# Kernel tuning notes

Measured on AMD Instinct MI355X. Metric: run time of the kernel, lower is better.

## Reference

```python
import jax, jax.numpy as jnp
import numpy as np


def _grid_sample_3d(vol, pts):
    """Trilinear grid_sample, align_corners=True, padding_mode='border'.
    vol: [C, D, H, W]; pts: [N, 3] with (x, y, z) in normalized [-1, 1] coords
    (x indexes W, y indexes H, z indexes D, matching torch.grid_sample).
    Returns [N, C]."""
    C, D, H, W = vol.shape
    def to_idx(c, size):
        c = (c + 1.0) * 0.5 * (size - 1)
        return jnp.clip(c, 0.0, size - 1.0)  # border padding
    ix = to_idx(pts[:, 0], W)
    iy = to_idx(pts[:, 1], H)
    iz = to_idx(pts[:, 2], D)
    x0 = jnp.floor(ix); y0 = jnp.floor(iy); z0 = jnp.floor(iz)
    wx = ix - x0;       wy = iy - y0;       wz = iz - z0
    x0i = x0.astype(jnp.int32); x1i = jnp.minimum(x0i + 1, W - 1)
    y0i = y0.astype(jnp.int32); y1i = jnp.minimum(y0i + 1, H - 1)
    z0i = z0.astype(jnp.int32); z1i = jnp.minimum(z0i + 1, D - 1)
    g = lambda zi, yi, xi: vol[:, zi, yi, xi]  # [C, N]
    out = (g(z0i, y0i, x0i) * (1 - wz) * (1 - wy) * (1 - wx)
         + g(z0i, y0i, x1i) * (1 - wz) * (1 - wy) * wx
         + g(z0i, y1i, x0i) * (1 - wz) * wy * (1 - wx)
         + g(z0i, y1i, x1i) * (1 - wz) * wy * wx
         + g(z1i, y0i, x0i) * wz * (1 - wy) * (1 - wx)
         + g(z1i, y0i, x1i) * wz * (1 - wy) * wx
         + g(z1i, y1i, x0i) * wz * wy * (1 - wx)
         + g(z1i, y1i, x1i) * wz * wy * wx)
    return out.T  # [N, C]


def _skinning(x, w, tfs):
    """x: [B,N,3], w: [B,N,J], tfs: [B,J,4,4] -> (xd [B,N,3], w_tf [B,N,4,4])."""
    x_h = jnp.concatenate([x, jnp.ones_like(x[..., :1])], axis=-1)  # [B,N,4]
    w_tf = jnp.einsum('bpn,bnij->bpij', w, tfs)                      # [B,N,4,4]
    xh = jnp.einsum('bpij,bpj->bpi', w_tf, x_h)                      # [B,N,4]
    return xh[..., :3], w_tf


def setup_inputs() -> dict:
    key = jax.random.key(0)
    ks = jax.random.split(key, 12)
    B, N, J = 4, 250000, 55
    return {
        'xc': jax.random.normal(ks[0], (B, N, 3), jnp.float32),
        'shape_offset': jax.random.normal(ks[1], (B, N, 3), jnp.float32),
        'pose_offset': jax.random.normal(ks[2], (B, N, 3), jnp.float32),
        'tfs': jax.random.normal(ks[3], (B, J, 4, 4), jnp.float32),
        'tfs_inv': jax.random.normal(ks[4], (1, J, 4, 4), jnp.float32),
        'poseoff_ori': jax.random.normal(ks[5], (1, N, 3), jnp.float32),
        'lbsw': jax.random.uniform(ks[6], (1, N, J), jnp.float32),
        'mask': jax.random.randint(ks[7], (1, N), 0, 2).astype(bool),
        'lbs_voxel': jax.random.uniform(ks[8], (1, J, 16, 64, 64), jnp.float32),
        'offset_kernel': jnp.zeros((1, 1, 3), jnp.float32),
        'scale_kernel': jax.random.uniform(ks[9], (1, 1, 3), jnp.float32),
    }


def reference(xc, shape_offset, pose_offset, tfs, tfs_inv, poseoff_ori,
              lbsw, mask, lbs_voxel, offset_kernel, scale_kernel):
    B = xc.shape[0]
    # query_weights: normalize then trilinear grid sample of shared voxel
    xn = (xc + offset_kernel) * scale_kernel  # [B,N,3]
    vol = lbs_voxel[0]                        # [J,16,64,64], shared across batch
    w = jax.vmap(lambda p: _grid_sample_3d(vol, p))(xn)  # [B,N,J]
    # w[:, mask[0]] = lbsw[mask]
    w = jnp.where(mask[0][None, :, None], lbsw, w)
    # first blend: canonical with tfs_inv (inverse=False path)
    xc_cano, w_tf_inv = _skinning(xc, w, jnp.broadcast_to(tfs_inv, (B,) + tfs_inv.shape[1:]))
    xc_cano_ori = xc_cano - poseoff_ori
    xc_shape = xc_cano_ori + shape_offset + pose_offset
    # second blend: posed with tfs
    xd, w_tf = _skinning(xc_shape, w, tfs)
    w_tf_all = w_tf @ w_tf_inv  # [B,N,4,4] batched 4x4 matmul
    return xd, w_tf_all
```

## Files before the change

kernel.cpp:

```cpp
#include <hip/hip_runtime.h>
#include <hip/hip_fp16.h>


#define JNT 55
#define VD  16
#define VH  64
#define VW  64
#define NVOX (VD * VH * VW)

typedef float f4u __attribute__((ext_vector_type(4), aligned(4)));

__global__ __launch_bounds__(256) void build_tab_k(
    const float* __restrict__ vol, const float* __restrict__ tfs,
    const float* __restrict__ tfs_inv, __half* __restrict__ tab)
{
    int v = blockIdx.x * 256 + threadIdx.x;
    int b = blockIdx.y;
    if (v >= NVOX) return;

    float Mi[16], Mv[16];
#pragma unroll
    for (int i = 0; i < 16; ++i) { Mi[i] = 0.f; Mv[i] = 0.f; }
    const float* tb = tfs + (size_t)b * JNT * 16;
#pragma unroll 1
    for (int j = 0; j < JNT; ++j) {
        float wj = vol[j * NVOX + v];
#pragma unroll
        for (int i = 0; i < 16; ++i) Mi[i] = fmaf(wj, tfs_inv[j * 16 + i], Mi[i]);
#pragma unroll
        for (int i = 0; i < 16; ++i) Mv[i] = fmaf(wj, tb[j * 16 + i], Mv[i]);
    }
    float h[16];
#pragma unroll
    for (int i = 0; i < 8; ++i)
        h[i] = __builtin_bit_cast(float, __floats2half2_rn(Mi[2*i], Mi[2*i+1]));
#pragma unroll
    for (int i = 0; i < 8; ++i)
        h[8+i] = __builtin_bit_cast(float, __floats2half2_rn(Mv[2*i], Mv[2*i+1]));

    float4* d4 = (float4*)(tab + ((size_t)b * NVOX + v) * 32);
    d4[0] = make_float4(h[0],  h[1],  h[2],  h[3]);
    d4[1] = make_float4(h[4],  h[5],  h[6],  h[7]);
    d4[2] = make_float4(h[8],  h[9],  h[10], h[11]);
    d4[3] = make_float4(h[12], h[13], h[14], h[15]);
}

__device__ __forceinline__ void acc8(float cw, float4 r, float* a)
{
    float rr[4] = {r.x, r.y, r.z, r.w};
#pragma unroll
    for (int kk = 0; kk < 4; ++kk) {
        __half2 h = __builtin_bit_cast(__half2, rr[kk]);
        float2 f = __half22float2(h);
        a[2*kk]     = fmaf(cw, f.x, a[2*kk]);
        a[2*kk + 1] = fmaf(cw, f.y, a[2*kk + 1]);
    }
}

__device__ __forceinline__ void epilogue(
    int b, int n, int N, float x, float y, float z,
    const float* A, const float* Ai,
    const float* __restrict__ shoff, const float* __restrict__ pooff,
    const float* __restrict__ poori,
    float* __restrict__ out_xd, float* __restrict__ out_w)
{
    size_t pid = (size_t)b * N + n;
    size_t p3  = pid * 3;
    size_t n3  = (size_t)n * 3;
    float c0 = Ai[0]*x + Ai[1]*y + Ai[2]*z  + Ai[3];
    float c1 = Ai[4]*x + Ai[5]*y + Ai[6]*z  + Ai[7];
    float c2 = Ai[8]*x + Ai[9]*y + Ai[10]*z + Ai[11];
    float sx = c0 - poori[n3 + 0] + shoff[p3 + 0] + pooff[p3 + 0];
    float sy = c1 - poori[n3 + 1] + shoff[p3 + 1] + pooff[p3 + 1];
    float sz = c2 - poori[n3 + 2] + shoff[p3 + 2] + pooff[p3 + 2];
    out_xd[p3 + 0] = A[0]*sx + A[1]*sy + A[2]*sz  + A[3];
    out_xd[p3 + 1] = A[4]*sx + A[5]*sy + A[6]*sz  + A[7];
    out_xd[p3 + 2] = A[8]*sx + A[9]*sy + A[10]*sz + A[11];

    float4* ow = (float4*)(out_w + pid * 16);
#pragma unroll
    for (int i = 0; i < 4; ++i) {
        float a0 = A[i*4+0], a1 = A[i*4+1], a2 = A[i*4+2], a3 = A[i*4+3];
        float4 r;
        r.x = a0*Ai[0] + a1*Ai[4] + a2*Ai[8]  + a3*Ai[12];
        r.y = a0*Ai[1] + a1*Ai[5] + a2*Ai[9]  + a3*Ai[13];
        r.z = a0*Ai[2] + a1*Ai[6] + a2*Ai[10] + a3*Ai[14];
        r.w = a0*Ai[3] + a1*Ai[7] + a2*Ai[11] + a3*Ai[15];
        ow[i] = r;
    }
}

template <int B>
__global__ __launch_bounds__(256) void main_k(
    const float* __restrict__ xc,
    const float* __restrict__ shoff,
    const float* __restrict__ pooff,
    const float* __restrict__ tfs,
    const float* __restrict__ tfs_inv,
    const float* __restrict__ poori,
    const float* __restrict__ lbsw,
    const int*   __restrict__ mask,
    const __half* __restrict__ tab,
    const float* __restrict__ offk,
    const float* __restrict__ sck,
    float* __restrict__ out_xd,
    float* __restrict__ out_w,
    int N)
{
    int tx = threadIdx.x;
    int ln = tx & 63;
    int b  = __builtin_amdgcn_readfirstlane(tx >> 6);
    int base = blockIdx.x * 64;

    int n0 = base + ln;
    bool mm = (n0 < N) && (mask[n0] != 0);
    unsigned long long bal = __ballot(mm);
    int nm = __popcll(bal);
    unsigned long long below = bal & ((1ull << ln) - 1ull);
    int rb = __popcll(below);
    int pos = mm ? rb : (nm + ln - rb);
    int slot = __builtin_amdgcn_ds_permute(pos << 2, ln);
    int n = base + slot;
    bool m = (ln < nm);
    if (n >= N) return;

    size_t p3 = ((size_t)b * N + n) * 3;
    float x = xc[p3], y = xc[p3 + 1], z = xc[p3 + 2];

    float A[16], Ai[16];
#pragma unroll
    for (int i = 0; i < 16; ++i) { A[i] = 0.f; Ai[i] = 0.f; }

    if (m) {
        const float* tb  = tfs + (size_t)b * JNT * 16;
        const float* row = lbsw + (size_t)n * JNT;
#pragma unroll 1
        for (int jj = 0; jj < 13; ++jj) {
            f4u w4 = *(const f4u*)(row + 4 * jj);
            float wq[4] = {w4.x, w4.y, w4.z, w4.w};
#pragma unroll
            for (int q = 0; q < 4; ++q) {
                int j = 4 * jj + q;
                float wj = wq[q];
#pragma unroll
                for (int i = 0; i < 16; ++i) Ai[i] = fmaf(wj, tfs_inv[j*16+i], Ai[i]);
#pragma unroll
                for (int i = 0; i < 16; ++i) A[i]  = fmaf(wj, tb[j*16+i],      A[i]);
            }
        }
#pragma unroll 1
        for (int j = 52; j < JNT; ++j) {
            float wj = row[j];
#pragma unroll
            for (int i = 0; i < 16; ++i) Ai[i] = fmaf(wj, tfs_inv[j*16+i], Ai[i]);
#pragma unroll
            for (int i = 0; i < 16; ++i) A[i]  = fmaf(wj, tb[j*16+i],      A[i]);
        }
    } else {
        float px = (x + offk[0]) * sck[0];
        float py = (y + offk[1]) * sck[1];
        float pz = (z + offk[2]) * sck[2];
        float ix = fminf(fmaxf((px + 1.f) * 0.5f * (VW - 1), 0.f), (float)(VW - 1));
        float iy = fminf(fmaxf((py + 1.f) * 0.5f * (VH - 1), 0.f), (float)(VH - 1));
        float iz = fminf(fmaxf((pz + 1.f) * 0.5f * (VD - 1), 0.f), (float)(VD - 1));
        float fx = floorf(ix), fy = floorf(iy), fz = floorf(iz);
        float wx = ix - fx,    wy = iy - fy,    wz = iz - fz;
        int x0 = (int)fx, y0 = (int)fy, z0 = (int)fz;
        int x1 = min(x0 + 1, VW - 1);
        int y1 = min(y0 + 1, VH - 1);
        int z1 = min(z0 + 1, VD - 1);

        const __half* tbb = tab + (size_t)b * NVOX * 32;
#pragma unroll 2
        for (int c = 0; c < 8; ++c) {
            int zc = (c & 4) ? z1 : z0;
            int yc = (c & 2) ? y1 : y0;
            int xcc = (c & 1) ? x1 : x0;
            float cw = ((c & 4) ? wz : 1.f - wz)
                     * ((c & 2) ? wy : 1.f - wy)
                     * ((c & 1) ? wx : 1.f - wx);
            int vox = (zc * VH + yc) * VW + xcc;
            const float4* e = (const float4*)(tbb + (size_t)vox * 32);
            float4 e0 = e[0], e1 = e[1], e2 = e[2], e3 = e[3];
            acc8(cw, e0, Ai);
            acc8(cw, e1, Ai + 8);
            acc8(cw, e2, A);
            acc8(cw, e3, A + 8);
        }
    }

    epilogue(b, n, N, x, y, z, A, Ai, shoff, pooff, poori, out_xd, out_w);
}

__global__ __launch_bounds__(256) void fb_k(
    const float* __restrict__ xc, const float* __restrict__ shoff,
    const float* __restrict__ pooff, const float* __restrict__ tfs,
    const float* __restrict__ tfs_inv, const float* __restrict__ poori,
    const float* __restrict__ lbsw, const int* __restrict__ mask,
    const float* __restrict__ vol, const float* __restrict__ offk,
    const float* __restrict__ sck, float* __restrict__ out_xd,
    float* __restrict__ out_w, int N)
{
    int n = blockIdx.x * 256 + threadIdx.x;
    int b = blockIdx.y;
    if (n >= N) return;
    size_t p3 = ((size_t)b * N + n) * 3;
    float x = xc[p3], y = xc[p3 + 1], z = xc[p3 + 2];
    float A[16], Ai[16];
#pragma unroll
    for (int i = 0; i < 16; ++i) { A[i] = 0.f; Ai[i] = 0.f; }
    const float* tb = tfs + (size_t)b * JNT * 16;

    if (mask[n] != 0) {
        const float* lp = lbsw + (size_t)n * JNT;
#pragma unroll 1
        for (int j = 0; j < JNT; ++j) {
            float wj = lp[j];
#pragma unroll
            for (int i = 0; i < 16; ++i) Ai[i] = fmaf(wj, tfs_inv[j*16+i], Ai[i]);
#pragma unroll
            for (int i = 0; i < 16; ++i) A[i]  = fmaf(wj, tb[j*16+i],      A[i]);
        }
    } else {
        float px = (x + offk[0]) * sck[0];
        float py = (y + offk[1]) * sck[1];
        float pz = (z + offk[2]) * sck[2];
        float ix = fminf(fmaxf((px + 1.f) * 0.5f * (VW - 1), 0.f), (float)(VW - 1));
        float iy = fminf(fmaxf((py + 1.f) * 0.5f * (VH - 1), 0.f), (float)(VH - 1));
        float iz = fminf(fmaxf((pz + 1.f) * 0.5f * (VD - 1), 0.f), (float)(VD - 1));
        float fx = floorf(ix), fy = floorf(iy), fz = floorf(iz);
        float wx = ix - fx, wy = iy - fy, wz = iz - fz;
        int x0 = (int)fx, y0 = (int)fy, z0 = (int)fz;
        int x1 = min(x0 + 1, VW - 1);
        int y1 = min(y0 + 1, VH - 1);
        int z1 = min(z0 + 1, VD - 1);
        float w00 = (1.f - wz) * (1.f - wy), w01 = (1.f - wz) * wy;
        float w10 = wz * (1.f - wy),         w11 = wz * wy;
        int o00 = (z0 * VH + y0) * VW, o01 = (z0 * VH + y1) * VW;
        int o10 = (z1 * VH + y0) * VW, o11 = (z1 * VH + y1) * VW;
#pragma unroll 1
        for (int j = 0; j < JNT; ++j) {
            const float* vp = vol + (size_t)j * NVOX;
            float v000 = vp[o00 + x0], v001 = vp[o00 + x1];
            float v010 = vp[o01 + x0], v011 = vp[o01 + x1];
            float v100 = vp[o10 + x0], v101 = vp[o10 + x1];
            float v110 = vp[o11 + x0], v111 = vp[o11 + x1];
            float c0 = w00 * v000 + w01 * v010 + w10 * v100 + w11 * v110;
            float c1 = w00 * v001 + w01 * v011 + w10 * v101 + w11 * v111;
            float wj = c0 + wx * (c1 - c0);
#pragma unroll
            for (int i = 0; i < 16; ++i) Ai[i] = fmaf(wj, tfs_inv[j*16+i], Ai[i]);
#pragma unroll
            for (int i = 0; i < 16; ++i) A[i]  = fmaf(wj, tb[j*16+i],      A[i]);
        }
    }
    epilogue(b, n, N, x, y, z, A, Ai, shoff, pooff, poori, out_xd, out_w);
}

extern "C" void kernel_launch(void* const* d_in, const int* in_sizes, int n_in,
                              void* d_out, int out_size, void* d_ws, size_t ws_size,
                              hipStream_t stream)
{
    const float* xc    = (const float*)d_in[0];
    const float* shoff = (const float*)d_in[1];
    const float* pooff = (const float*)d_in[2];
    const float* tfs   = (const float*)d_in[3];
    const float* tfsi  = (const float*)d_in[4];
    const float* poori = (const float*)d_in[5];
    const float* lbsw  = (const float*)d_in[6];
    const int*   mask  = (const int*)d_in[7];
    const float* vol   = (const float*)d_in[8];
    const float* offk  = (const float*)d_in[9];
    const float* sck   = (const float*)d_in[10];

    int N = in_sizes[5] / 3;
    int B = in_sizes[0] / (3 * N);
    float* out_xd = (float*)d_out;
    float* out_w  = (float*)d_out + (size_t)B * N * 3;

    size_t tab_bytes = (size_t)B * NVOX * 32 * sizeof(__half);
    __half* tab = (__half*)d_ws;

    if (B == 4 && ws_size >= tab_bytes) {
        build_tab_k<<<dim3((NVOX + 255) / 256, 4), dim3(256), 0, stream>>>(
            vol, tfs, tfsi, tab);
        main_k<4><<<dim3((N + 63) / 64), dim3(256), 0, stream>>>(
            xc, shoff, pooff, tfs, tfsi, poori, lbsw, mask, tab,
            offk, sck, out_xd, out_w, N);
    } else {
        fb_k<<<dim3((N + 255) / 256, B), dim3(256), 0, stream>>>(
            xc, shoff, pooff, tfs, tfsi, poori, lbsw, mask, vol, offk, sck,
            out_xd, out_w, N);
    }
}
```

Before: 278.0 us.

## Compact masked points across 256-point block via shared-memory permutation

Each block now covers 256 points instead of 64. Masked and unmasked points are sorted across the whole block with a shared-memory prefix scan, and each wave loops over four 64-point chunks of the permuted order. This cuts warp divergence between the lbsw-blend path and the voxel-table path, since fewer wavefronts hold both kinds of point. In exchange it adds two block barriers and a serial loop per wave, and it launches a quarter as many blocks.

```diff
diff --git a/kernel.cpp b/kernel.cpp
--- a/kernel.cpp
+++ b/kernel.cpp
@@ -107,89 +107,112 @@
     float* __restrict__ out_w,
     int N)
 {
+    __shared__ unsigned short sPerm[256];
+    __shared__ int sCnt[4];
+
     int tx = threadIdx.x;
     int ln = tx & 63;
-    int b  = __builtin_amdgcn_readfirstlane(tx >> 6);
-    int base = blockIdx.x * 64;
-
-    int n0 = base + ln;
-    bool mm = (n0 < N) && (mask[n0] != 0);
-    unsigned long long bal = __ballot(mm);
-    int nm = __popcll(bal);
-    unsigned long long below = bal & ((1ull << ln) - 1ull);
-    int rb = __popcll(below);
-    int pos = mm ? rb : (nm + ln - rb);
-    int slot = __builtin_amdgcn_ds_permute(pos << 2, ln);
-    int n = base + slot;
-    bool m = (ln < nm);
-    if (n >= N) return;
-
-    size_t p3 = ((size_t)b * N + n) * 3;
-    float x = xc[p3], y = xc[p3 + 1], z = xc[p3 + 2];
-
-    float A[16], Ai[16];
-#pragma unroll
-    for (int i = 0; i < 16; ++i) { A[i] = 0.f; Ai[i] = 0.f; }
-
-    if (m) {
-        const float* tb  = tfs + (size_t)b * JNT * 16;
-        const float* row = lbsw + (size_t)n * JNT;
-#pragma unroll 1
-        for (int jj = 0; jj < 13; ++jj) {
-            f4u w4 = *(const f4u*)(row + 4 * jj);
-            float wq[4] = {w4.x, w4.y, w4.z, w4.w};
-#pragma unroll
-            for (int q = 0; q < 4; ++q) {
-                int j = 4 * jj + q;
-                float wj = wq[q];
+    int wv = tx >> 6;
+    int b  = __builtin_amdgcn_readfirstlane(wv);
+    int base = blockIdx.x * 256;
+
+    {
+        int n0 = base + tx;
+        bool mm = (n0 < N) && (mask[n0] != 0);
+        unsigned long long bal = __ballot(mm);
+        int cm = __popcll(bal);
+        if (ln == 0) sCnt[wv] = cm;
+        __syncthreads();
+        int c0 = sCnt[0], c1 = sCnt[1], c2 = sCnt[2], c3 = sCnt[3];
+        int totM  = c0 + c1 + c2 + c3;
+        int mBase = (wv > 0 ? c0 : 0) + (wv > 1 ? c1 : 0) + (wv > 2 ? c2 : 0);
+        unsigned long long below = bal & ((1ull << ln) - 1ull);
+        int rm  = __popcll(below);
+        int pos = mm ? (mBase + rm) : (totM + (wv * 64 - mBase) + (ln - rm));
+        sPerm[pos] = (unsigned short)tx;
+        if (tx == 0) sCnt[0] = totM;
+        __syncthreads();
+    }
+    int totM = sCnt[0];
+
+    float o0 = offk[0], o1 = offk[1], o2 = offk[2];
+    float s0 = sck[0],  s1 = sck[1],  s2 = sck[2];
+    const float*  tb  = tfs + (size_t)b * JNT * 16;
+    const __half* tbb = tab + (size_t)b * NVOX * 32;
+
+#pragma unroll 1
+    for (int c = 0; c < 4; ++c) {
+        int r   = c * 64 + ln;
+        int slot = sPerm[r];
+        int n = base + slot;
+        bool m = (r < totM);
+        if (n >= N) continue;
+
+        size_t p3 = ((size_t)b * N + n) * 3;
+        float x = xc[p3], y = xc[p3 + 1], z = xc[p3 + 2];
+
+        float A[16], Ai[16];
+#pragma unroll
+        for (int i = 0; i < 16; ++i) { A[i] = 0.f; Ai[i] = 0.f; }
+
+        if (m) {
+            const float* row = lbsw + (size_t)n * JNT;
+#pragma unroll 1
+            for (int jj = 0; jj < 13; ++jj) {
+                f4u w4 = *(const f4u*)(row + 4 * jj);
+                float wq[4] = {w4.x, w4.y, w4.z, w4.w};
+#pragma unroll
+                for (int q = 0; q < 4; ++q) {
+                    int j = 4 * jj + q;
+                    float wj = wq[q];
+#pragma unroll
+                    for (int i = 0; i < 16; ++i) Ai[i] = fmaf(wj, tfs_inv[j*16+i], Ai[i]);
+#pragma unroll
+                    for (int i = 0; i < 16; ++i) A[i]  = fmaf(wj, tb[j*16+i],      A[i]);
+                }
+            }
+#pragma unroll 1
+            for (int j = 52; j < JNT; ++j) {
+                float wj = row[j];
 #pragma unroll
                 for (int i = 0; i < 16; ++i) Ai[i] = fmaf(wj, tfs_inv[j*16+i], Ai[i]);
 #pragma unroll
                 for (int i = 0; i < 16; ++i) A[i]  = fmaf(wj, tb[j*16+i],      A[i]);
             }
+        } else {
+            float px = (x + o0) * s0;
+            float py = (y + o1) * s1;
+            float pz = (z + o2) * s2;
+            float ix = fminf(fmaxf((px + 1.f) * 0.5f * (VW - 1), 0.f), (float)(VW - 1));
+            float iy = fminf(fmaxf((py + 1.f) * 0.5f * (VH - 1), 0.f), (float)(VH - 1));
+            float iz = fminf(fmaxf((pz + 1.f) * 0.5f * (VD - 1), 0.f), (float)(VD - 1));
+            float fx = floorf(ix), fy = floorf(iy), fz = floorf(iz);
+            float wx = ix - fx,    wy = iy - fy,    wz = iz - fz;
+            int x0 = (int)fx, y0 = (int)fy, z0 = (int)fz;
+            int x1 = min(x0 + 1, VW - 1);
+            int y1 = min(y0 + 1, VH - 1);
+            int z1 = min(z0 + 1, VD - 1);
+
+#pragma unroll 2
+            for (int cc = 0; cc < 8; ++cc) {
+                int zc  = (cc & 4) ? z1 : z0;
+                int yc  = (cc & 2) ? y1 : y0;
+                int xcc = (cc & 1) ? x1 : x0;
+                float cw = ((cc & 4) ? wz : 1.f - wz)
+                         * ((cc & 2) ? wy : 1.f - wy)
+                         * ((cc & 1) ? wx : 1.f - wx);
+                int vox = (zc * VH + yc) * VW + xcc;
+                const float4* e = (const float4*)(tbb + (size_t)vox * 32);
+                float4 e0 = e[0], e1 = e[1], e2 = e[2], e3 = e[3];
+                acc8(cw, e0, Ai);
+                acc8(cw, e1, Ai + 8);
+                acc8(cw, e2, A);
+                acc8(cw, e3, A + 8);
+            }
         }
-#pragma unroll 1
-        for (int j = 52; j < JNT; ++j) {
-            float wj = row[j];
-#pragma unroll
-            for (int i = 0; i < 16; ++i) Ai[i] = fmaf(wj, tfs_inv[j*16+i], Ai[i]);
-#pragma unroll
-            for (int i = 0; i < 16; ++i) A[i]  = fmaf(wj, tb[j*16+i],      A[i]);
-        }
-    } else {
-        float px = (x + offk[0]) * sck[0];
-        float py = (y + offk[1]) * sck[1];
-        float pz = (z + offk[2]) * sck[2];
-        float ix = fminf(fmaxf((px + 1.f) * 0.5f * (VW - 1), 0.f), (float)(VW - 1));
-        float iy = fminf(fmaxf((py + 1.f) * 0.5f * (VH - 1), 0.f), (float)(VH - 1));
-        float iz = fminf(fmaxf((pz + 1.f) * 0.5f * (VD - 1), 0.f), (float)(VD - 1));
-        float fx = floorf(ix), fy = floorf(iy), fz = floorf(iz);
-        float wx = ix - fx,    wy = iy - fy,    wz = iz - fz;
-        int x0 = (int)fx, y0 = (int)fy, z0 = (int)fz;
-        int x1 = min(x0 + 1, VW - 1);
-        int y1 = min(y0 + 1, VH - 1);
-        int z1 = min(z0 + 1, VD - 1);
-
-        const __half* tbb = tab + (size_t)b * NVOX * 32;
-#pragma unroll 2
-        for (int c = 0; c < 8; ++c) {
-            int zc = (c & 4) ? z1 : z0;
-            int yc = (c & 2) ? y1 : y0;
-            int xcc = (c & 1) ? x1 : x0;
-            float cw = ((c & 4) ? wz : 1.f - wz)
-                     * ((c & 2) ? wy : 1.f - wy)
-                     * ((c & 1) ? wx : 1.f - wx);
-            int vox = (zc * VH + yc) * VW + xcc;
-            const float4* e = (const float4*)(tbb + (size_t)vox * 32);
-            float4 e0 = e[0], e1 = e[1], e2 = e[2], e3 = e[3];
-            acc8(cw, e0, Ai);
-            acc8(cw, e1, Ai + 8);
-            acc8(cw, e2, A);
-            acc8(cw, e3, A + 8);
-        }
-    }
-
-    epilogue(b, n, N, x, y, z, A, Ai, shoff, pooff, poori, out_xd, out_w);
+
+        epilogue(b, n, N, x, y, z, A, Ai, shoff, pooff, poori, out_xd, out_w);
+    }
 }
 
 __global__ __launch_bounds__(256) void fb_k(
@@ -284,7 +307,7 @@
     if (B == 4 && ws_size >= tab_bytes) {
         build_tab_k<<<dim3((NVOX + 255) / 256, 4), dim3(256), 0, stream>>>(
             vol, tfs, tfsi, tab);
-        main_k<4><<<dim3((N + 63) / 64), dim3(256), 0, stream>>>(
+        main_k<4><<<dim3((N + 255) / 256), dim3(256), 0, stream>>>(
             xc, shoff, pooff, tfs, tfsi, poori, lbsw, mask, tab,
             offk, sck, out_xd, out_w, N);
     } else {
```

Result: slower. 308.8 us (+11.1%).
